# Performance work log

Hardware: AMD Instinct MI355X
Metric: run time of the kernel (lower is better)

Reference implementation:

```python
import jax, jax.numpy as jnp
import numpy as np

N_NODES = 50000
N_EDGES = 400000
D_IN = 128
D_H = 128
N_CLASSES = 20
N_GRAPHS = 256
EPS_BN = 1e-5


def _lin_params(key, d_in, d_out, scale=0.05):
    kw, kb = jax.random.split(key)
    W = jax.random.normal(kw, (d_in, d_out), jnp.float32) * scale
    b = jax.random.normal(kb, (d_out,), jnp.float32) * scale
    return W, b


def setup_inputs() -> dict:
    key = jax.random.key(0)
    ks = jax.random.split(key, 20)
    inp = {
        "x": jax.random.normal(ks[0], (N_NODES, D_IN), jnp.float32),
        "edge_index": jax.random.randint(ks[1], (2, N_EDGES), 0, N_NODES, jnp.int32),
        "batch": jnp.sort(jax.random.randint(ks[2], (N_NODES,), 0, N_GRAPHS, jnp.int32)),
    }
    kidx = 3
    for li, d_in in zip((1, 2, 3), (D_IN, D_H, D_H)):
        for nm in ("q", "k", "v", "s"):
            W, b = _lin_params(ks[kidx], d_in, D_H)
            kidx += 1
            inp[f"W{nm}{li}"] = W
            inp[f"b{nm}{li}"] = b
        inp[f"gamma{li}"] = jnp.ones((D_H,), jnp.float32)
        inp[f"beta{li}"] = jnp.zeros((D_H,), jnp.float32)
    Wl, bl = _lin_params(ks[kidx], D_H, N_CLASSES)
    inp["Wlin"] = Wl
    inp["blin"] = bl
    return inp


def _segment_softmax(logits, seg, n):
    m = jax.ops.segment_max(logits, seg, num_segments=n)
    e = jnp.exp(logits - m[seg])
    s = jax.ops.segment_sum(e, seg, num_segments=n)
    return e / (s[seg] + 1e-16)


def _transformer_conv(x, src, dst, Wq, bq, Wk, bk, Wv, bv, Ws, bs):
    # heads=1, concat=True, root_weight=True (PyG TransformerConv defaults)
    q = x @ Wq + bq  # [N, d]
    k = x @ Wk + bk
    v = x @ Wv + bv
    d = q.shape[-1]
    logits = jnp.sum(q[dst] * k[src], axis=-1) / jnp.sqrt(jnp.float32(d))  # [E]
    alpha = _segment_softmax(logits, dst, x.shape[0])
    out = jax.ops.segment_sum(alpha[:, None] * v[src], dst, num_segments=x.shape[0])
    return out + x @ Ws + bs


def _batch_norm(x, gamma, beta):
    mu = jnp.mean(x, axis=0)
    var = jnp.var(x, axis=0)
    return gamma * (x - mu) * jax.lax.rsqrt(var + EPS_BN) + beta


def _global_mean_pool(x, batch, n_graphs):
    sums = jax.ops.segment_sum(x, batch, num_segments=n_graphs)
    cnt = jax.ops.segment_sum(jnp.ones((x.shape[0],), x.dtype), batch, num_segments=n_graphs)
    return sums / jnp.maximum(cnt, 1.0)[:, None]


def reference(x, edge_index, batch,
              Wq1, bq1, Wk1, bk1, Wv1, bv1, Ws1, bs1, gamma1, beta1,
              Wq2, bq2, Wk2, bk2, Wv2, bv2, Ws2, bs2, gamma2, beta2,
              Wq3, bq3, Wk3, bk3, Wv3, bv3, Ws3, bs3, gamma3, beta3,
              Wlin, blin):
    src, dst = edge_index[0], edge_index[1]
    h = _transformer_conv(x, src, dst, Wq1, bq1, Wk1, bk1, Wv1, bv1, Ws1, bs1)
    h = jax.nn.relu(_batch_norm(h, gamma1, beta1))  # dropout inactive (eval)
    h = _transformer_conv(h, src, dst, Wq2, bq2, Wk2, bk2, Wv2, bv2, Ws2, bs2)
    h = jax.nn.relu(_batch_norm(h, gamma2, beta2))
    h = _transformer_conv(h, src, dst, Wq3, bq3, Wk3, bk3, Wv3, bv3, Ws3, bs3)
    h = jax.nn.relu(_batch_norm(h, gamma3, beta3))
    g = _global_mean_pool(h, batch, N_GRAPHS)  # [G, d]
    return g @ Wlin + blin  # [G, num_classes]
```

## Files before the change

### kernel.cpp

```cpp
#include <hip/hip_runtime.h>

#define N_NODES 50000
#define N_EDGES 400000
#define DH 128
#define N_GRAPHS 256

#define SCAN_CHUNK 512
#define N_CHUNKS ((N_NODES + SCAN_CHUNK - 1) / SCAN_CHUNK)
#define ATTN_BLOCKS ((N_NODES + 7) / 8)
#define POOL_CHUNKS ((N_NODES + 63) / 64)

typedef __bf16 bf16x8 __attribute__((ext_vector_type(8)));
typedef float f32x4 __attribute__((ext_vector_type(4)));
typedef _Float16 f16x4 __attribute__((ext_vector_type(4)));
typedef _Float16 f16x8 __attribute__((ext_vector_type(8)));

#define DEV __device__ __forceinline__

DEV unsigned short f2bf(float f) {
  union { float f; unsigned int i; } v; v.f = f;
  unsigned int x = v.i;
  unsigned int r = (x + 0x7fffu + ((x >> 16) & 1u)) >> 16;
  return (unsigned short)r;
}

struct WPtrs { const float* w[12]; };

__global__ void repack_kernel(WPtrs wp, unsigned short* __restrict__ WB) {
  int mat = blockIdx.y;
  int m = blockIdx.x * 256 + threadIdx.x;
  int j = m & 7;
  int lane = (m >> 3) & 63;
  int ct = (m >> 9) & 7;
  int kk = m >> 12;
  int i = kk * 32 + (lane >> 4) * 8 + j;
  int o = ct * 16 + (lane & 15);
  WB[mat * 16384 + m] = f2bf(wp.w[mat][i * 128 + o]);
}

__global__ void f32_to_bf16(const float* __restrict__ in, unsigned short* __restrict__ out,
                            int total4) {
  int i = blockIdx.x * 256 + threadIdx.x;
  if (i >= total4) return;
  float4 v = *reinterpret_cast<const float4*>(in + i * 4);
  ushort4 o;
  o.x = f2bf(v.x); o.y = f2bf(v.y); o.z = f2bf(v.z); o.w = f2bf(v.w);
  *reinterpret_cast<ushort4*>(out + i * 4) = o;
}

__global__ void deg_count(const int* __restrict__ ei, int* __restrict__ deg, int E) {
  int e = blockIdx.x * 256 + threadIdx.x;
  if (e < E) atomicAdd(&deg[ei[E + e]], 1);
}

__global__ __launch_bounds__(256) void scan_sum(const int* __restrict__ deg,
                                                int* __restrict__ partials, int N) {
  __shared__ int red[256];
  int b = blockIdx.x, t = threadIdx.x;
  int base = b * SCAN_CHUNK + t * 2;
  int s = 0;
  if (base + 1 < N) { int2 v = *reinterpret_cast<const int2*>(deg + base); s = v.x + v.y; }
  else if (base < N) s = deg[base];
  red[t] = s;
  __syncthreads();
  for (int off = 128; off; off >>= 1) {
    if (t < off) red[t] += red[t + off];
    __syncthreads();
  }
  if (t == 0) partials[b] = red[0];
}

__global__ __launch_bounds__(128) void scan_partials(int* __restrict__ partials) {
  __shared__ int s[128];
  int t = threadIdx.x;
  int v = (t < N_CHUNKS) ? partials[t] : 0;
  s[t] = v;
  __syncthreads();
  for (int off = 1; off < 128; off <<= 1) {
    int o = (t >= off) ? s[t - off] : 0;
    __syncthreads();
    s[t] += o;
    __syncthreads();
  }
  if (t < N_CHUNKS) partials[t] = s[t] - v;
}

__global__ __launch_bounds__(256) void scan_apply(const int* __restrict__ deg,
                                                  const int* __restrict__ partials,
                                                  int* __restrict__ rowptr,
                                                  int* __restrict__ cursor, int N, int E) {
  __shared__ int s[256];
  int b = blockIdx.x, t = threadIdx.x;
  int base = b * SCAN_CHUNK + t * 2;
  int d0 = 0, d1 = 0;
  if (base + 1 < N) { int2 v = *reinterpret_cast<const int2*>(deg + base); d0 = v.x; d1 = v.y; }
  else if (base < N) d0 = deg[base];
  int local = d0 + d1;
  s[t] = local;
  __syncthreads();
  for (int off = 1; off < 256; off <<= 1) {
    int o = (t >= off) ? s[t - off] : 0;
    __syncthreads();
    s[t] += o;
    __syncthreads();
  }
  int offp = partials[b] + s[t] - local;
  if (base < N)     { rowptr[base] = offp;          cursor[base] = offp; }
  if (base + 1 < N) { rowptr[base + 1] = offp + d0; cursor[base + 1] = offp + d0; }
  if (b == 0 && t == 0) rowptr[N] = E;
}

__global__ void csr_scatter(const int* __restrict__ ei, int* __restrict__ cursor,
                            int* __restrict__ adj, int E) {
  int e = blockIdx.x * 256 + threadIdx.x;
  if (e < E) {
    int dst = ei[E + e];
    int pos = atomicAdd(&cursor[dst], 1);
    adj[pos] = ei[e];
  }
}

struct GemmOut { _Float16* Y[4]; const float* bias[4]; };

#define LDP 136

__global__ __launch_bounds__(256) void gemm_proj(
    const unsigned short* __restrict__ X,
    const _Float16* __restrict__ Hin,
    const float* __restrict__ scale, const float* __restrict__ shift,
    const unsigned short* __restrict__ WB4,
    GemmOut go, int useBN, int N)
{
  __shared__ __align__(16) unsigned short xs[64 * LDP];

  const int t = threadIdx.x;
  const int rowBase = blockIdx.x * 64;
  const int igc = (t & 15) * 8;

  if (useBN) {
    float4 sc0 = *reinterpret_cast<const float4*>(scale + igc);
    float4 sc1 = *reinterpret_cast<const float4*>(scale + igc + 4);
    float4 sh0 = *reinterpret_cast<const float4*>(shift + igc);
    float4 sh1 = *reinterpret_cast<const float4*>(shift + igc + 4);
#pragma unroll
    for (int j = 0; j < 4; ++j) {
      int v = t + 256 * j;
      int r = v >> 4;
      int grow = rowBase + r;
      ushort4 o0 = make_ushort4(0, 0, 0, 0), o1 = make_ushort4(0, 0, 0, 0);
      if (grow < N) {
        f16x8 hv = *reinterpret_cast<const f16x8*>(Hin + (size_t)grow * 128 + igc);
        o0.x = f2bf(fmaxf((float)hv[0] * sc0.x + sh0.x, 0.f));
        o0.y = f2bf(fmaxf((float)hv[1] * sc0.y + sh0.y, 0.f));
        o0.z = f2bf(fmaxf((float)hv[2] * sc0.z + sh0.z, 0.f));
        o0.w = f2bf(fmaxf((float)hv[3] * sc0.w + sh0.w, 0.f));
        o1.x = f2bf(fmaxf((float)hv[4] * sc1.x + sh1.x, 0.f));
        o1.y = f2bf(fmaxf((float)hv[5] * sc1.y + sh1.y, 0.f));
        o1.z = f2bf(fmaxf((float)hv[6] * sc1.z + sh1.z, 0.f));
        o1.w = f2bf(fmaxf((float)hv[7] * sc1.w + sh1.w, 0.f));
      }
      *reinterpret_cast<ushort4*>(&xs[r * LDP + igc]) = o0;
      *reinterpret_cast<ushort4*>(&xs[r * LDP + igc + 4]) = o1;
    }
  } else {
#pragma unroll
    for (int j = 0; j < 4; ++j) {
      int v = t + 256 * j;
      int r = v >> 4;
      int grow = rowBase + r;
      uint4 val = make_uint4(0u, 0u, 0u, 0u);
      if (grow < N) val = *reinterpret_cast<const uint4*>(X + (size_t)grow * 128 + igc);
      *reinterpret_cast<uint4*>(&xs[r * LDP + igc]) = val;
    }
  }
  __syncthreads();

  const int wave = t >> 6;
  const int lane = t & 63;
  const int ln16 = lane & 15;
  const int quad = lane >> 4;
  const int r0 = wave * 16;

  bf16x8 afrag[4];
#pragma unroll
  for (int kk = 0; kk < 4; ++kk)
    afrag[kk] = *reinterpret_cast<const bf16x8*>(&xs[(r0 + ln16) * LDP + kk * 32 + quad * 8]);

  for (int proj = 0; proj < 4; ++proj) {
    const unsigned short* __restrict__ WB = WB4 + proj * 16384;
    const float* __restrict__ bias = go.bias[proj];

    f32x4 acc[8] = {};
#pragma unroll
    for (int kk = 0; kk < 4; ++kk) {
#pragma unroll
      for (int ct = 0; ct < 8; ++ct) {
        bf16x8 b = *reinterpret_cast<const bf16x8*>(WB + ((kk * 8 + ct) * 64 + lane) * 8);
        acc[ct] = __builtin_amdgcn_mfma_f32_16x16x32_bf16(afrag[kk], b, acc[ct], 0, 0, 0);
      }
    }

    _Float16* __restrict__ Yh = go.Y[proj];
#pragma unroll
    for (int ct = 0; ct < 8; ++ct) {
      int col = ct * 16 + ln16;
      float bv = bias[col];
#pragma unroll
      for (int reg = 0; reg < 4; ++reg) {
        int grow = rowBase + r0 + quad * 4 + reg;
        if (grow < N) Yh[(size_t)grow * 128 + col] = (_Float16)(acc[ct][reg] + bv);
      }
    }
  }
}

__global__ __launch_bounds__(256) void node_attn(
    const int* __restrict__ rowptr, const int* __restrict__ adj,
    const _Float16* __restrict__ Q, const _Float16* __restrict__ K,
    const _Float16* __restrict__ V, _Float16* __restrict__ H,
    float* __restrict__ Pbuf, int N)
{
  __shared__ float lsum[8][128];
  __shared__ float lsq[8][128];
  int t = threadIdx.x;
  int w = t >> 5, lane = t & 31;
  int n = blockIdx.x * 8 + w;
  bool valid = n < N;
  int nn = valid ? n : 0;
  int p0 = 0, p1 = 0;
  if (valid) { p0 = rowptr[n]; p1 = rowptr[n + 1]; }

  f16x4 qh = *reinterpret_cast<const f16x4*>(Q + (size_t)nn * 128 + lane * 4);
  float4 q = make_float4((float)qh.x, (float)qh.y, (float)qh.z, (float)qh.w);
  float m = -INFINITY, s = 0.f;
  float4 acc = make_float4(0.f, 0.f, 0.f, 0.f);

  int p = p0;
  for (; p + 1 < p1; p += 2) {
    int s0 = adj[p], s1 = adj[p + 1];
    f16x4 k0 = *reinterpret_cast<const f16x4*>(K + (size_t)s0 * 128 + lane * 4);
    f16x4 k1 = *reinterpret_cast<const f16x4*>(K + (size_t)s1 * 128 + lane * 4);
    float d0 = q.x * (float)k0.x + q.y * (float)k0.y + q.z * (float)k0.z + q.w * (float)k0.w;
    float d1 = q.x * (float)k1.x + q.y * (float)k1.y + q.z * (float)k1.z + q.w * (float)k1.w;
#pragma unroll
    for (int off = 16; off; off >>= 1) {
      d0 += __shfl_xor(d0, off, 32);
      d1 += __shfl_xor(d1, off, 32);
    }
    float l0 = d0 * 0.08838834764831845f;
    float l1 = d1 * 0.08838834764831845f;
    float mn = fmaxf(m, fmaxf(l0, l1));
    float sc = __expf(m - mn);
    float w0 = __expf(l0 - mn);
    float w1 = __expf(l1 - mn);
    f16x4 v0 = *reinterpret_cast<const f16x4*>(V + (size_t)s0 * 128 + lane * 4);
    f16x4 v1 = *reinterpret_cast<const f16x4*>(V + (size_t)s1 * 128 + lane * 4);
    acc.x = acc.x * sc + w0 * (float)v0.x + w1 * (float)v1.x;
    acc.y = acc.y * sc + w0 * (float)v0.y + w1 * (float)v1.y;
    acc.z = acc.z * sc + w0 * (float)v0.z + w1 * (float)v1.z;
    acc.w = acc.w * sc + w0 * (float)v0.w + w1 * (float)v1.w;
    s = s * sc + w0 + w1;
    m = mn;
  }
  if (p < p1) {
    int s0 = adj[p];
    f16x4 k0 = *reinterpret_cast<const f16x4*>(K + (size_t)s0 * 128 + lane * 4);
    float d0 = q.x * (float)k0.x + q.y * (float)k0.y + q.z * (float)k0.z + q.w * (float)k0.w;
#pragma unroll
    for (int off = 16; off; off >>= 1) d0 += __shfl_xor(d0, off, 32);
    float l0 = d0 * 0.08838834764831845f;
    float mn = fmaxf(m, l0);
    float sc = __expf(m - mn);
    float w0 = __expf(l0 - mn);
    f16x4 v0 = *reinterpret_cast<const f16x4*>(V + (size_t)s0 * 128 + lane * 4);
    acc.x = acc.x * sc + w0 * (float)v0.x;
    acc.y = acc.y * sc + w0 * (float)v0.y;
    acc.z = acc.z * sc + w0 * (float)v0.z;
    acc.w = acc.w * sc + w0 * (float)v0.w;
    s = s * sc + w0;
    m = mn;
  }

  float4 h = make_float4(0.f, 0.f, 0.f, 0.f);
  if (valid) {
    float inv = 1.0f / (s + 1e-16f);
    f16x4 hh = *reinterpret_cast<const f16x4*>(H + (size_t)n * 128 + lane * 4);
    h.x = (float)hh.x + acc.x * inv;
    h.y = (float)hh.y + acc.y * inv;
    h.z = (float)hh.z + acc.z * inv;
    h.w = (float)hh.w + acc.w * inv;
    f16x4 ho;
    ho.x = (_Float16)h.x; ho.y = (_Float16)h.y; ho.z = (_Float16)h.z; ho.w = (_Float16)h.w;
    *reinterpret_cast<f16x4*>(H + (size_t)n * 128 + lane * 4) = ho;
  }

  *reinterpret_cast<float4*>(&lsum[w][lane * 4]) = h;
  float4 h2 = make_float4(h.x * h.x, h.y * h.y, h.z * h.z, h.w * h.w);
  *reinterpret_cast<float4*>(&lsq[w][lane * 4]) = h2;
  __syncthreads();

  int f = t & 127;
  float a = 0.f;
  if (t < 128) {
#pragma unroll
    for (int n8 = 0; n8 < 8; ++n8) a += lsum[n8][f];
  } else {
#pragma unroll
    for (int n8 = 0; n8 < 8; ++n8) a += lsq[n8][f];
  }
  Pbuf[(size_t)blockIdx.x * 256 + t] = a;
}

__global__ __launch_bounds__(256) void bn_reduceA(const float* __restrict__ Pbuf,
                                                  float* __restrict__ partial) {
  int t = threadIdx.x;
  float s0 = 0.f, s1 = 0.f, s2 = 0.f, s3 = 0.f;
  int r = blockIdx.x;
  for (; r + 192 < ATTN_BLOCKS; r += 256) {
    s0 += Pbuf[(size_t)(r      ) * 256 + t];
    s1 += Pbuf[(size_t)(r +  64) * 256 + t];
    s2 += Pbuf[(size_t)(r + 128) * 256 + t];
    s3 += Pbuf[(size_t)(r + 192) * 256 + t];
  }
  for (; r < ATTN_BLOCKS; r += 64) s0 += Pbuf[(size_t)r * 256 + t];
  partial[blockIdx.x * 256 + t] = s0 + s1 + s2 + s3;
}

__global__ __launch_bounds__(256) void bn_reduceB(
    const float* __restrict__ partial,
    const float* __restrict__ gamma, const float* __restrict__ beta,
    float* __restrict__ scale, float* __restrict__ shift, int N)
{
  __shared__ float red[256];
  int t = threadIdx.x;
  float s0 = 0.f, s1 = 0.f, s2 = 0.f, s3 = 0.f;
#pragma unroll
  for (int r = 0; r < 64; r += 4) {
    s0 += partial[(r + 0) * 256 + t];
    s1 += partial[(r + 1) * 256 + t];
    s2 += partial[(r + 2) * 256 + t];
    s3 += partial[(r + 3) * 256 + t];
  }
  red[t] = s0 + s1 + s2 + s3;
  __syncthreads();
  if (t < 128) {
    float mean = red[t] / (float)N;
    float var = red[t + 128] / (float)N - mean * mean;
    var = fmaxf(var, 0.f);
    float sc = gamma[t] * rsqrtf(var + 1e-5f);
    scale[t] = sc;
    shift[t] = beta[t] - mean * sc;
  }
}

__global__ __launch_bounds__(256) void pool_chunk(
    const _Float16* __restrict__ H, const float* __restrict__ scale,
    const float* __restrict__ shift, const int* __restrict__ batch,
    float* __restrict__ pooled, int N)
{
  int f = threadIdx.x & 127, half = threadIdx.x >> 7;
  int base = blockIdx.x * 64;
  int lim = min(base + 64, N);
  float sc = scale[f], sh = shift[f];
  int curg = -1; float s = 0.f;
  for (int row = base + half; row < lim; row += 2) {
    int g = batch[row];
    if (g != curg) {
      if (curg >= 0) unsafeAtomicAdd(pooled + curg * 128 + f, s);
      curg = g; s = 0.f;
    }
    s += fmaxf((float)H[(size_t)row * 128 + f] * sc + sh, 0.f);
  }
  if (curg >= 0) unsafeAtomicAdd(pooled + curg * 128 + f, s);
}

__global__ __launch_bounds__(64) void final_linear(
    const float* __restrict__ pooled, const int* __restrict__ batch,
    const float* __restrict__ Wlin, const float* __restrict__ blin,
    float* __restrict__ out, int N)
{
  int g = blockIdx.x;
  int c = threadIdx.x;
  int lo = 0, hi = N;
  while (lo < hi) { int mid = (lo + hi) >> 1; if (batch[mid] < g) lo = mid + 1; else hi = mid; }
  int start = lo;
  hi = N;
  while (lo < hi) { int mid = (lo + hi) >> 1; if (batch[mid] < g + 1) lo = mid + 1; else hi = mid; }
  float inv = 1.0f / fmaxf((float)(lo - start), 1.f);
  if (c < 20) {
    float acc = 0.f;
#pragma unroll 4
    for (int i = 0; i < 128; ++i)
      acc += pooled[g * 128 + i] * Wlin[i * 20 + c];
    out[g * 20 + c] = acc * inv + blin[c];
  }
}

extern "C" void kernel_launch(void* const* d_in, const int* in_sizes, int n_in,
                              void* d_out, int out_size, void* d_ws, size_t ws_size,
                              hipStream_t stream)
{
  const int N = N_NODES, E = N_EDGES, G = N_GRAPHS;

  const float* x = (const float*)d_in[0];
  const int* ei = (const int*)d_in[1];
  const int* batch = (const int*)d_in[2];
  const float* Wlin = (const float*)d_in[33];
  const float* blin = (const float*)d_in[34];

  char* ws = (char*)d_ws;
  size_t off = 0;
  auto alloc = [&](size_t bytes) -> void* {
    void* p = ws + off;
    off = (off + bytes + 255) & ~(size_t)255;
    return p;
  };
  unsigned short* WB = (unsigned short*)alloc(12 * 16384 * sizeof(unsigned short));
  _Float16* Qh  = (_Float16*)alloc((size_t)N * 128 * 2);
  _Float16* Kh  = (_Float16*)alloc((size_t)N * 128 * 2);
  _Float16* Vh  = (_Float16*)alloc((size_t)N * 128 * 2);
  _Float16* Hh  = (_Float16*)alloc((size_t)N * 128 * 2);
  int* deg      = (int*)alloc((size_t)N * 4);
  int* rowptr   = (int*)alloc((size_t)(N + 1) * 4);
  int* cursor   = (int*)alloc((size_t)N * 4);
  int* adj      = (int*)alloc((size_t)E * 4);
  int* partials = (int*)alloc((size_t)N_CHUNKS * 4);
  float* Pbuf   = (float*)alloc((size_t)ATTN_BLOCKS * 256 * 4);
  float* bnpart = (float*)alloc((size_t)64 * 256 * 4);
  float* scale  = (float*)alloc(128 * 4);
  float* shift  = (float*)alloc(128 * 4);
  float* pooled = (float*)alloc((size_t)G * 128 * 4);
  unsigned short* Xb = (unsigned short*)alloc((size_t)N * 128 * 2);

  WPtrs wp;
  for (int L = 0; L < 3; ++L) {
    wp.w[L * 4 + 0] = (const float*)d_in[3 + L * 10 + 0];
    wp.w[L * 4 + 1] = (const float*)d_in[3 + L * 10 + 2];
    wp.w[L * 4 + 2] = (const float*)d_in[3 + L * 10 + 4];
    wp.w[L * 4 + 3] = (const float*)d_in[3 + L * 10 + 6];
  }
  repack_kernel<<<dim3(64, 12), 256, 0, stream>>>(wp, WB);
  f32_to_bf16<<<(N * 128 / 4 + 255) / 256, 256, 0, stream>>>(x, Xb, N * 128 / 4);

  hipMemsetAsync(deg, 0, (size_t)N * 4, stream);
  deg_count<<<(E + 255) / 256, 256, 0, stream>>>(ei, deg, E);
  scan_sum<<<N_CHUNKS, 256, 0, stream>>>(deg, partials, N);
  scan_partials<<<1, 128, 0, stream>>>(partials);
  scan_apply<<<N_CHUNKS, 256, 0, stream>>>(deg, partials, rowptr, cursor, N, E);
  csr_scatter<<<(E + 255) / 256, 256, 0, stream>>>(ei, cursor, adj, E);

  for (int L = 0; L < 3; ++L) {
    GemmOut go;
    go.Y[0] = Qh; go.Y[1] = Kh; go.Y[2] = Vh; go.Y[3] = Hh;
    go.bias[0] = (const float*)d_in[3 + L * 10 + 1];
    go.bias[1] = (const float*)d_in[3 + L * 10 + 3];
    go.bias[2] = (const float*)d_in[3 + L * 10 + 5];
    go.bias[3] = (const float*)d_in[3 + L * 10 + 7];
    gemm_proj<<<(N + 63) / 64, 256, 0, stream>>>(
        Xb, Hh, scale, shift, WB + L * 4 * 16384, go, (L > 0) ? 1 : 0, N);

    node_attn<<<ATTN_BLOCKS, 256, 0, stream>>>(rowptr, adj, Qh, Kh, Vh, Hh, Pbuf, N);

    bn_reduceA<<<64, 256, 0, stream>>>(Pbuf, bnpart);
    bn_reduceB<<<1, 256, 0, stream>>>(bnpart,
        (const float*)d_in[3 + L * 10 + 8],
        (const float*)d_in[3 + L * 10 + 9],
        scale, shift, N);

    if (L == 2) {
      hipMemsetAsync(pooled, 0, (size_t)G * 128 * 4, stream);
      pool_chunk<<<POOL_CHUNKS, 256, 0, stream>>>(Hh, scale, shift, batch, pooled, N);
      final_linear<<<G, 64, 0, stream>>>(pooled, batch, Wlin, blin, (float*)d_out, N);
    }
  }
}
```

Baseline: 479.7 us.

## Use 16-lane groups per node with fdot2, fuse input bf16 conversion into GEMM

```diff
diff --git a/kernel.cpp b/kernel.cpp
--- a/kernel.cpp
+++ b/kernel.cpp
@@ -7,15 +7,29 @@
 
 #define SCAN_CHUNK 512
 #define N_CHUNKS ((N_NODES + SCAN_CHUNK - 1) / SCAN_CHUNK)
-#define ATTN_BLOCKS ((N_NODES + 7) / 8)
+#define ATTN_BLOCKS ((N_NODES + 15) / 16)
 #define POOL_CHUNKS ((N_NODES + 63) / 64)
 
 typedef __bf16 bf16x8 __attribute__((ext_vector_type(8)));
 typedef float f32x4 __attribute__((ext_vector_type(4)));
-typedef _Float16 f16x4 __attribute__((ext_vector_type(4)));
+typedef _Float16 f16x2 __attribute__((ext_vector_type(2)));
 typedef _Float16 f16x8 __attribute__((ext_vector_type(8)));
 
 #define DEV __device__ __forceinline__
+
+#if defined(__has_builtin)
+#if __has_builtin(__builtin_amdgcn_fdot2)
+#define HAS_FDOT2 1
+#endif
+#endif
+
+DEV float fdot2acc(f16x2 a, f16x2 b, float c) {
+#ifdef HAS_FDOT2
+  return __builtin_amdgcn_fdot2(a, b, c, false);
+#else
+  return (float)a.x * (float)b.x + (float)a.y * (float)b.y + c;
+#endif
+}
 
 DEV unsigned short f2bf(float f) {
   union { float f; unsigned int i; } v; v.f = f;
@@ -36,16 +50,6 @@
   int i = kk * 32 + (lane >> 4) * 8 + j;
   int o = ct * 16 + (lane & 15);
   WB[mat * 16384 + m] = f2bf(wp.w[mat][i * 128 + o]);
-}
-
-__global__ void f32_to_bf16(const float* __restrict__ in, unsigned short* __restrict__ out,
-                            int total4) {
-  int i = blockIdx.x * 256 + threadIdx.x;
-  if (i >= total4) return;
-  float4 v = *reinterpret_cast<const float4*>(in + i * 4);
-  ushort4 o;
-  o.x = f2bf(v.x); o.y = f2bf(v.y); o.z = f2bf(v.z); o.w = f2bf(v.w);
-  *reinterpret_cast<ushort4*>(out + i * 4) = o;
 }
 
 __global__ void deg_count(const int* __restrict__ ei, int* __restrict__ deg, int E) {
@@ -125,7 +129,7 @@
 #define LDP 136
 
 __global__ __launch_bounds__(256) void gemm_proj(
-    const unsigned short* __restrict__ X,
+    const float* __restrict__ Xf,
     const _Float16* __restrict__ Hin,
     const float* __restrict__ scale, const float* __restrict__ shift,
     const unsigned short* __restrict__ WB4,
@@ -168,9 +172,15 @@
       int v = t + 256 * j;
       int r = v >> 4;
       int grow = rowBase + r;
-      uint4 val = make_uint4(0u, 0u, 0u, 0u);
-      if (grow < N) val = *reinterpret_cast<const uint4*>(X + (size_t)grow * 128 + igc);
-      *reinterpret_cast<uint4*>(&xs[r * LDP + igc]) = val;
+      ushort4 o0 = make_ushort4(0, 0, 0, 0), o1 = make_ushort4(0, 0, 0, 0);
+      if (grow < N) {
+        float4 a = *reinterpret_cast<const float4*>(Xf + (size_t)grow * 128 + igc);
+        float4 b = *reinterpret_cast<const float4*>(Xf + (size_t)grow * 128 + igc + 4);
+        o0.x = f2bf(a.x); o0.y = f2bf(a.y); o0.z = f2bf(a.z); o0.w = f2bf(a.w);
+        o1.x = f2bf(b.x); o1.y = f2bf(b.y); o1.z = f2bf(b.z); o1.w = f2bf(b.w);
+      }
+      *reinterpret_cast<ushort4*>(&xs[r * LDP + igc]) = o0;
+      *reinterpret_cast<ushort4*>(&xs[r * LDP + igc + 4]) = o1;
     }
   }
   __syncthreads();
@@ -220,32 +230,39 @@
     const _Float16* __restrict__ V, _Float16* __restrict__ H,
     float* __restrict__ Pbuf, int N)
 {
-  __shared__ float lsum[8][128];
-  __shared__ float lsq[8][128];
+  __shared__ float lsum[16][128];
+  __shared__ float lsq[16][128];
   int t = threadIdx.x;
-  int w = t >> 5, lane = t & 31;
-  int n = blockIdx.x * 8 + w;
+  int w = t >> 4, lane = t & 15;
+  int n = blockIdx.x * 16 + w;
   bool valid = n < N;
   int nn = valid ? n : 0;
   int p0 = 0, p1 = 0;
   if (valid) { p0 = rowptr[n]; p1 = rowptr[n + 1]; }
 
-  f16x4 qh = *reinterpret_cast<const f16x4*>(Q + (size_t)nn * 128 + lane * 4);
-  float4 q = make_float4((float)qh.x, (float)qh.y, (float)qh.z, (float)qh.w);
+  f16x8 qv = *reinterpret_cast<const f16x8*>(Q + (size_t)nn * 128 + lane * 8);
+  f16x2 q0 = {qv[0], qv[1]}, q1 = {qv[2], qv[3]}, q2 = {qv[4], qv[5]}, q3 = {qv[6], qv[7]};
+
   float m = -INFINITY, s = 0.f;
-  float4 acc = make_float4(0.f, 0.f, 0.f, 0.f);
+  float acc[8] = {};
 
   int p = p0;
   for (; p + 1 < p1; p += 2) {
     int s0 = adj[p], s1 = adj[p + 1];
-    f16x4 k0 = *reinterpret_cast<const f16x4*>(K + (size_t)s0 * 128 + lane * 4);
-    f16x4 k1 = *reinterpret_cast<const f16x4*>(K + (size_t)s1 * 128 + lane * 4);
-    float d0 = q.x * (float)k0.x + q.y * (float)k0.y + q.z * (float)k0.z + q.w * (float)k0.w;
-    float d1 = q.x * (float)k1.x + q.y * (float)k1.y + q.z * (float)k1.z + q.w * (float)k1.w;
-#pragma unroll
-    for (int off = 16; off; off >>= 1) {
-      d0 += __shfl_xor(d0, off, 32);
-      d1 += __shfl_xor(d1, off, 32);
+    f16x8 k0 = *reinterpret_cast<const f16x8*>(K + (size_t)s0 * 128 + lane * 8);
+    f16x8 k1 = *reinterpret_cast<const f16x8*>(K + (size_t)s1 * 128 + lane * 8);
+    float d0 = fdot2acc(q0, (f16x2){k0[0], k0[1]},
+               fdot2acc(q1, (f16x2){k0[2], k0[3]},
+               fdot2acc(q2, (f16x2){k0[4], k0[5]},
+               fdot2acc(q3, (f16x2){k0[6], k0[7]}, 0.f))));
+    float d1 = fdot2acc(q0, (f16x2){k1[0], k1[1]},
+               fdot2acc(q1, (f16x2){k1[2], k1[3]},
+               fdot2acc(q2, (f16x2){k1[4], k1[5]},
+               fdot2acc(q3, (f16x2){k1[6], k1[7]}, 0.f))));
+#pragma unroll
+    for (int off = 8; off; off >>= 1) {
+      d0 += __shfl_xor(d0, off, 16);
+      d1 += __shfl_xor(d1, off, 16);
     }
     float l0 = d0 * 0.08838834764831845f;
     float l1 = d1 * 0.08838834764831845f;
@@ -253,60 +270,67 @@
     float sc = __expf(m - mn);
     float w0 = __expf(l0 - mn);
     float w1 = __expf(l1 - mn);
-    f16x4 v0 = *reinterpret_cast<const f16x4*>(V + (size_t)s0 * 128 + lane * 4);
-    f16x4 v1 = *reinterpret_cast<const f16x4*>(V + (size_t)s1 * 128 + lane * 4);
-    acc.x = acc.x * sc + w0 * (float)v0.x + w1 * (float)v1.x;
-    acc.y = acc.y * sc + w0 * (float)v0.y + w1 * (float)v1.y;
-    acc.z = acc.z * sc + w0 * (float)v0.z + w1 * (float)v1.z;
-    acc.w = acc.w * sc + w0 * (float)v0.w + w1 * (float)v1.w;
+    f16x8 v0 = *reinterpret_cast<const f16x8*>(V + (size_t)s0 * 128 + lane * 8);
+    f16x8 v1 = *reinterpret_cast<const f16x8*>(V + (size_t)s1 * 128 + lane * 8);
+#pragma unroll
+    for (int i = 0; i < 8; ++i)
+      acc[i] = acc[i] * sc + w0 * (float)v0[i] + w1 * (float)v1[i];
     s = s * sc + w0 + w1;
     m = mn;
   }
   if (p < p1) {
     int s0 = adj[p];
-    f16x4 k0 = *reinterpret_cast<const f16x4*>(K + (size_t)s0 * 128 + lane * 4);
-    float d0 = q.x * (float)k0.x + q.y * (float)k0.y + q.z * (float)k0.z + q.w * (float)k0.w;
-#pragma unroll
-    for (int off = 16; off; off >>= 1) d0 += __shfl_xor(d0, off, 32);
+    f16x8 k0 = *reinterpret_cast<const f16x8*>(K + (size_t)s0 * 128 + lane * 8);
+    float d0 = fdot2acc(q0, (f16x2){k0[0], k0[1]},
+               fdot2acc(q1, (f16x2){k0[2], k0[3]},
+               fdot2acc(q2, (f16x2){k0[4], k0[5]},
+               fdot2acc(q3, (f16x2){k0[6], k0[7]}, 0.f))));
+#pragma unroll
+    for (int off = 8; off; off >>= 1) d0 += __shfl_xor(d0, off, 16);
     float l0 = d0 * 0.08838834764831845f;
     float mn = fmaxf(m, l0);
     float sc = __expf(m - mn);
     float w0 = __expf(l0 - mn);
-    f16x4 v0 = *reinterpret_cast<const f16x4*>(V + (size_t)s0 * 128 + lane * 4);
-    acc.x = acc.x * sc + w0 * (float)v0.x;
-    acc.y = acc.y * sc + w0 * (float)v0.y;
-    acc.z = acc.z * sc + w0 * (float)v0.z;
-    acc.w = acc.w * sc + w0 * (float)v0.w;
+    f16x8 v0 = *reinterpret_cast<const f16x8*>(V + (size_t)s0 * 128 + lane * 8);
+#pragma unroll
+    for (int i = 0; i < 8; ++i)
+      acc[i] = acc[i] * sc + w0 * (float)v0[i];
     s = s * sc + w0;
     m = mn;
   }
 
-  float4 h = make_float4(0.f, 0.f, 0.f, 0.f);
+  float h[8];
+#pragma unroll
+  for (int i = 0; i < 8; ++i) h[i] = 0.f;
   if (valid) {
     float inv = 1.0f / (s + 1e-16f);
-    f16x4 hh = *reinterpret_cast<const f16x4*>(H + (size_t)n * 128 + lane * 4);
-    h.x = (float)hh.x + acc.x * inv;
-    h.y = (float)hh.y + acc.y * inv;
-    h.z = (float)hh.z + acc.z * inv;
-    h.w = (float)hh.w + acc.w * inv;
-    f16x4 ho;
-    ho.x = (_Float16)h.x; ho.y = (_Float16)h.y; ho.z = (_Float16)h.z; ho.w = (_Float16)h.w;
-    *reinterpret_cast<f16x4*>(H + (size_t)n * 128 + lane * 4) = ho;
-  }
-
-  *reinterpret_cast<float4*>(&lsum[w][lane * 4]) = h;
-  float4 h2 = make_float4(h.x * h.x, h.y * h.y, h.z * h.z, h.w * h.w);
-  *reinterpret_cast<float4*>(&lsq[w][lane * 4]) = h2;
+    f16x8 hh = *reinterpret_cast<const f16x8*>(H + (size_t)n * 128 + lane * 8);
+    f16x8 ho;
+#pragma unroll
+    for (int i = 0; i < 8; ++i) {
+      h[i] = (float)hh[i] + acc[i] * inv;
+      ho[i] = (_Float16)h[i];
+    }
+    *reinterpret_cast<f16x8*>(H + (size_t)n * 128 + lane * 8) = ho;
+  }
+
+#pragma unroll
+  for (int i = 0; i < 8; i += 4) {
+    float4 hv = make_float4(h[i], h[i + 1], h[i + 2], h[i + 3]);
+    float4 h2 = make_float4(hv.x * hv.x, hv.y * hv.y, hv.z * hv.z, hv.w * hv.w);
+    *reinterpret_cast<float4*>(&lsum[w][lane * 8 + i]) = hv;
+    *reinterpret_cast<float4*>(&lsq[w][lane * 8 + i]) = h2;
+  }
   __syncthreads();
 
   int f = t & 127;
   float a = 0.f;
   if (t < 128) {
 #pragma unroll
-    for (int n8 = 0; n8 < 8; ++n8) a += lsum[n8][f];
+    for (int n16 = 0; n16 < 16; ++n16) a += lsum[n16][f];
   } else {
 #pragma unroll
-    for (int n8 = 0; n8 < 8; ++n8) a += lsq[n8][f];
+    for (int n16 = 0; n16 < 16; ++n16) a += lsq[n16][f];
   }
   Pbuf[(size_t)blockIdx.x * 256 + t] = a;
 }
@@ -430,7 +454,6 @@
   float* scale  = (float*)alloc(128 * 4);
   float* shift  = (float*)alloc(128 * 4);
   float* pooled = (float*)alloc((size_t)G * 128 * 4);
-  unsigned short* Xb = (unsigned short*)alloc((size_t)N * 128 * 2);
 
   WPtrs wp;
   for (int L = 0; L < 3; ++L) {
@@ -440,7 +463,6 @@
     wp.w[L * 4 + 3] = (const float*)d_in[3 + L * 10 + 6];
   }
   repack_kernel<<<dim3(64, 12), 256, 0, stream>>>(wp, WB);
-  f32_to_bf16<<<(N * 128 / 4 + 255) / 256, 256, 0, stream>>>(x, Xb, N * 128 / 4);
 
   hipMemsetAsync(deg, 0, (size_t)N * 4, stream);
   deg_count<<<(E + 255) / 256, 256, 0, stream>>>(ei, deg, E);
@@ -457,7 +479,7 @@
     go.bias[2] = (const float*)d_in[3 + L * 10 + 5];
     go.bias[3] = (const float*)d_in[3 + L * 10 + 7];
     gemm_proj<<<(N + 63) / 64, 256, 0, stream>>>(
-        Xb, Hh, scale, shift, WB + L * 4 * 16384, go, (L > 0) ? 1 : 0, N);
+        x, Hh, scale, shift, WB + L * 4 * 16384, go, (L > 0) ? 1 : 0, N);
 
     node_attn<<<ATTN_BLOCKS, 256, 0, stream>>>(rowptr, adj, Qh, Kh, Vh, Hh, Pbuf, N);
 
```

Result: faster. 446.0 us (-7.0%).
